# Performance work log

Hardware: AMD Instinct MI355X
Metric: run time of the kernel (lower is better)

The kernel has to match this reference:

```python
import jax, jax.numpy as jnp
import numpy as np
import math

HID = 4096
SLOTS = 8
HEADS = 8
BD = 512  # bottleneck_dim
HD = BD // HEADS  # effective head dim = 64
B, S = 4, 4096


def setup_inputs() -> dict:
    key = jax.random.key(0)
    ks = jax.random.split(key, 8)
    std = 1.0 / math.sqrt(HID)
    return {
        "hidden_states": jax.random.normal(ks[0], (B, S, HID), dtype=jnp.float32),
        "attention_mask": jax.random.randint(ks[1], (B, S), 0, 2, dtype=jnp.int32),
        "memory_slots": jax.random.normal(ks[2], (SLOTS, HID), dtype=jnp.float32) * std,
        # torch nn.Linear weights are [out_features, in_features]
        "Wq": jax.random.normal(ks[3], (BD, HID), dtype=jnp.float32) * std,
        "Wk": jax.random.normal(ks[4], (BD, HID), dtype=jnp.float32) * std,
        "Wv": jax.random.normal(ks[5], (BD, HID), dtype=jnp.float32) * std,
        "Wo": jax.random.normal(ks[6], (HID, BD), dtype=jnp.float32) * (1.0 / math.sqrt(BD)),
    }


def reference(hidden_states, attention_mask, memory_slots, Wq, Wk, Wv, Wo):
    # Q from learnable slots (same for every batch element): [slots, BD]
    Q = memory_slots @ Wq.T
    Q = Q.reshape(SLOTS, HEADS, HD)                      # n h d
    # K/V from sequence: [b, s, BD] -> [b, s, h, d]
    K = jnp.einsum('bsi,oi->bso', hidden_states, Wk).reshape(B, S, HEADS, HD)
    V = jnp.einsum('bsi,oi->bso', hidden_states, Wv).reshape(B, S, HEADS, HD)
    # scores: [b, h, n, s]
    scores = jnp.einsum('nhd,bshd->bhns', Q, K) / jnp.sqrt(jnp.array(HD, scores_dtype := jnp.float32))
    mask = attention_mask[:, None, None, :]              # [b,1,1,s]
    scores = jnp.where(mask == 0, jnp.finfo(scores.dtype).min, scores)
    attn = jax.nn.softmax(scores, axis=-1)
    # output: [b, n, h, d] -> [b, n, BD]
    out = jnp.einsum('bhns,bshd->bnhd', attn, V).reshape(B, SLOTS, BD)
    # o_proj back to hidden_size
    return jnp.einsum('bnd,od->bno', out, Wo)            # [b, slots, HID]
```

## Files before the change

### kernel.cpp

```cpp
#include <hip/hip_runtime.h>
#include <math.h>

#define HID   4096
#define SLOTS 8
#define HEADS 8
#define BD    512
#define HD    64
#define BB    4
#define SS    4096
#define R64   64
#define LSTR  72

typedef __attribute__((ext_vector_type(8))) short bf16x8;
typedef __attribute__((ext_vector_type(4))) float f32x4;

__device__ __forceinline__ unsigned short f2bf(float x) {
  unsigned int u = __builtin_bit_cast(unsigned int, x);
  return (unsigned short)((u + 0x7fffu + ((u >> 16) & 1u)) >> 16);
}

__global__ void q_kernel(const float* __restrict__ ms, const float* __restrict__ Wq,
                         float* __restrict__ Q) {
  int w = (blockIdx.x * blockDim.x + threadIdx.x) >> 6;
  int lane = threadIdx.x & 63;
  if (w >= SLOTS * BD) return;
  int n = w >> 9, o = w & (BD - 1);
  const float* a = ms + n * HID;
  const float* b = Wq + (size_t)o * HID;
  float acc = 0.f;
  for (int i = lane; i < HID; i += 64) acc = fmaf(a[i], b[i], acc);
  #pragma unroll
  for (int off = 32; off; off >>= 1) acc += __shfl_down(acc, off, 64);
  if (lane == 0) Q[w] = acc;
}

__global__ void qw_kernel(const float* __restrict__ Q, const float* __restrict__ Wk,
                          unsigned short* __restrict__ QW) {
  int idx = blockIdx.x * blockDim.x + threadIdx.x;
  int r = idx >> 12, i = idx & (HID - 1);
  int h = r >> 3, n = r & 7;
  const float* q  = Q + n * BD + h * HD;
  const float* wk = Wk + (size_t)(h * HD) * HID + i;
  float acc = 0.f;
  #pragma unroll 8
  for (int d = 0; d < HD; ++d) acc = fmaf(q[d], wk[(size_t)d * HID], acc);
  QW[idx] = f2bf(acc * 0.125f);
}

__global__ __launch_bounds__(256) void scores_mfma(const float* __restrict__ hs,
                                                   const unsigned short* __restrict__ QW,
                                                   float* __restrict__ sp) {
  __shared__ unsigned short As[64 * LSTR];
  __shared__ unsigned short Bs[64 * LSTR];
  const int stile = blockIdx.x, b = blockIdx.y;
  const int tid = threadIdx.x;
  const int wv = tid >> 6, lane = tid & 63;
  const int quad = lane >> 4, l16 = lane & 15;
  const int srow = tid >> 2, kc = (tid & 3) << 4;
  const float* hsp = hs + ((size_t)(b * SS + stile * 64 + srow)) * HID + kc;
  const unsigned short* qwp = QW + (size_t)srow * HID + kc;

  f32x4 acc[4] = {};
  float4 fa0 = *(const float4*)(hsp + 0);
  float4 fa1 = *(const float4*)(hsp + 4);
  float4 fa2 = *(const float4*)(hsp + 8);
  float4 fa3 = *(const float4*)(hsp + 12);
  uint4 qb0 = *(const uint4*)(qwp);
  uint4 qb1 = *(const uint4*)(qwp + 8);

  for (int c = 0; c < 64; ++c) {
    __syncthreads();
    union { unsigned short us[16]; uint4 q[2]; } u;
    float f[16] = {fa0.x, fa0.y, fa0.z, fa0.w, fa1.x, fa1.y, fa1.z, fa1.w,
                   fa2.x, fa2.y, fa2.z, fa2.w, fa3.x, fa3.y, fa3.z, fa3.w};
    #pragma unroll
    for (int j = 0; j < 16; ++j) u.us[j] = f2bf(f[j]);
    *(uint4*)&As[srow * LSTR + kc]     = u.q[0];
    *(uint4*)&As[srow * LSTR + kc + 8] = u.q[1];
    *(uint4*)&Bs[srow * LSTR + kc]     = qb0;
    *(uint4*)&Bs[srow * LSTR + kc + 8] = qb1;
    __syncthreads();
    if (c < 63) {
      const float* p = hsp + (size_t)(c + 1) * 64;
      fa0 = *(const float4*)(p + 0);
      fa1 = *(const float4*)(p + 4);
      fa2 = *(const float4*)(p + 8);
      fa3 = *(const float4*)(p + 12);
      const unsigned short* q = qwp + (size_t)(c + 1) * 64;
      qb0 = *(const uint4*)(q);
      qb1 = *(const uint4*)(q + 8);
    }
    #pragma unroll
    for (int ks = 0; ks < 2; ++ks) {
      bf16x8 bfrag = *(const bf16x8*)&Bs[(wv * 16 + l16) * LSTR + ks * 32 + quad * 8];
      #pragma unroll
      for (int mt = 0; mt < 4; ++mt) {
        bf16x8 afrag = *(const bf16x8*)&As[(mt * 16 + l16) * LSTR + ks * 32 + quad * 8];
        acc[mt] = __builtin_amdgcn_mfma_f32_16x16x32_bf16(afrag, bfrag, acc[mt], 0, 0, 0);
      }
    }
  }
  const int r = wv * 16 + l16;
  #pragma unroll
  for (int mt = 0; mt < 4; ++mt) {
    int s = stile * 64 + mt * 16 + quad * 4;
    float4 v = make_float4(acc[mt][0], acc[mt][1], acc[mt][2], acc[mt][3]);
    *(float4*)(sp + ((size_t)(b * R64 + r)) * SS + s) = v;
  }
}

__global__ __launch_bounds__(256) void softmax_kernel(const float* __restrict__ sp,
                                                      const int* __restrict__ mask,
                                                      unsigned short* __restrict__ attn) {
  int br = blockIdx.x;
  int b = br >> 6;
  int tid = threadIdx.x;
  const float* row = sp + (size_t)br * SS;
  const int* mrow = mask + b * SS;
  float vals[16];
  float mx = -INFINITY;
  #pragma unroll
  for (int j = 0; j < 16; ++j) {
    int s = tid + j * 256;
    float v = row[s];
    if (mrow[s] == 0) v = -INFINITY;
    vals[j] = v;
    mx = fmaxf(mx, v);
  }
  __shared__ float redm[4], reds[4];
  #pragma unroll
  for (int off = 32; off; off >>= 1) mx = fmaxf(mx, __shfl_down(mx, off, 64));
  if ((tid & 63) == 0) redm[tid >> 6] = mx;
  __syncthreads();
  mx = fmaxf(fmaxf(redm[0], redm[1]), fmaxf(redm[2], redm[3]));
  float sum = 0.f;
  #pragma unroll
  for (int j = 0; j < 16; ++j) { vals[j] = expf(vals[j] - mx); sum += vals[j]; }
  #pragma unroll
  for (int off = 32; off; off >>= 1) sum += __shfl_down(sum, off, 64);
  if ((tid & 63) == 0) reds[tid >> 6] = sum;
  __syncthreads();
  sum = reds[0] + reds[1] + reds[2] + reds[3];
  float inv = 1.f / sum;
  #pragma unroll
  for (int j = 0; j < 16; ++j)
    attn[(size_t)br * SS + tid + j * 256] = f2bf(vals[j] * inv);
}

__global__ __launch_bounds__(256) void ctx_mfma(const unsigned short* __restrict__ attn,
                                                const float* __restrict__ hs,
                                                float* __restrict__ ctx) {
  __shared__ unsigned short As[64 * LSTR];
  __shared__ unsigned short Bs[64 * LSTR];
  const int itile = blockIdx.x, b = blockIdx.y;
  const int tid = threadIdx.x;
  const int wv = tid >> 6, lane = tid & 63;
  const int quad = lane >> 4, l16 = lane & 15;
  const int arow = tid >> 2, asc = (tid & 3) << 4;
  const unsigned short* ap = attn + ((size_t)(b * R64 + arow)) * SS + asc;
  const int p = tid & 31, g = tid >> 5;
  const float* bp0 = hs + ((size_t)(b * SS + 2 * p)) * HID + itile * 64 + g * 8;
  const float* bp1 = bp0 + HID;

  f32x4 acc[4] = {};
  uint4 aa0 = *(const uint4*)(ap);
  uint4 aa1 = *(const uint4*)(ap + 8);
  float4 hb00 = *(const float4*)(bp0);
  float4 hb01 = *(const float4*)(bp0 + 4);
  float4 hb10 = *(const float4*)(bp1);
  float4 hb11 = *(const float4*)(bp1 + 4);

  for (int c = 0; c < 64; ++c) {
    __syncthreads();
    *(uint4*)&As[arow * LSTR + asc]     = aa0;
    *(uint4*)&As[arow * LSTR + asc + 8] = aa1;
    {
      float lo[8] = {hb00.x, hb00.y, hb00.z, hb00.w, hb01.x, hb01.y, hb01.z, hb01.w};
      float hi[8] = {hb10.x, hb10.y, hb10.z, hb10.w, hb11.x, hb11.y, hb11.z, hb11.w};
      #pragma unroll
      for (int j = 0; j < 8; ++j) {
        unsigned int v = (unsigned int)f2bf(lo[j]) | ((unsigned int)f2bf(hi[j]) << 16);
        ((unsigned int*)Bs)[(g * 8 + j) * (LSTR / 2) + p] = v;
      }
    }
    __syncthreads();
    if (c < 63) {
      const unsigned short* an = ap + (size_t)(c + 1) * 64;
      aa0 = *(const uint4*)(an);
      aa1 = *(const uint4*)(an + 8);
      const float* bn0 = bp0 + (size_t)(c + 1) * 64 * HID;
      const float* bn1 = bn0 + HID;
      hb00 = *(const float4*)(bn0);
      hb01 = *(const float4*)(bn0 + 4);
      hb10 = *(const float4*)(bn1);
      hb11 = *(const float4*)(bn1 + 4);
    }
    #pragma unroll
    for (int ks = 0; ks < 2; ++ks) {
      bf16x8 bfrag = *(const bf16x8*)&Bs[(wv * 16 + l16) * LSTR + ks * 32 + quad * 8];
      #pragma unroll
      for (int mt = 0; mt < 4; ++mt) {
        bf16x8 afrag = *(const bf16x8*)&As[(mt * 16 + l16) * LSTR + ks * 32 + quad * 8];
        acc[mt] = __builtin_amdgcn_mfma_f32_16x16x32_bf16(afrag, bfrag, acc[mt], 0, 0, 0);
      }
    }
  }
  const int i = itile * 64 + wv * 16 + l16;
  #pragma unroll
  for (int mt = 0; mt < 4; ++mt) {
    int r0 = mt * 16 + quad * 4;
    #pragma unroll
    for (int j = 0; j < 4; ++j)
      ctx[((size_t)(b * R64 + r0 + j)) * HID + i] = acc[mt][j];
  }
}

__global__ void out_kernel(const float* __restrict__ ctx, const float* __restrict__ Wv,
                           float* __restrict__ out) {
  int w = (blockIdx.x * blockDim.x + threadIdx.x) >> 6;
  int lane = threadIdx.x & 63;
  if (w >= BB * SLOTS * BD) return;
  int b = w >> 12, n = (w >> 9) & 7, hd = w & 511, h = hd >> 6;
  const float* c  = ctx + ((size_t)b * R64 + h * 8 + n) * HID;
  const float* wv = Wv + (size_t)hd * HID;
  float acc = 0.f;
  for (int i = lane; i < HID; i += 64) acc = fmaf(c[i], wv[i], acc);
  #pragma unroll
  for (int off = 32; off; off >>= 1) acc += __shfl_down(acc, off, 64);
  if (lane == 0) out[w] = acc;
}

__global__ void final_kernel(const float* __restrict__ out, const float* __restrict__ Wo,
                             float* __restrict__ y) {
  int w = (blockIdx.x * blockDim.x + threadIdx.x) >> 6;
  int lane = threadIdx.x & 63;
  if (w >= BB * SLOTS * HID) return;
  int bn = w >> 12, o = w & 4095;
  const float* orow = out + bn * BD;
  const float* wo = Wo + (size_t)o * BD;
  float acc = 0.f;
  #pragma unroll
  for (int d = lane; d < BD; d += 64) acc = fmaf(orow[d], wo[d], acc);
  #pragma unroll
  for (int off = 32; off; off >>= 1) acc += __shfl_down(acc, off, 64);
  if (lane == 0) y[w] = acc;
}

extern "C" void kernel_launch(void* const* d_in, const int* in_sizes, int n_in,
                              void* d_out, int out_size, void* d_ws, size_t ws_size,
                              hipStream_t stream) {
  const float* hs   = (const float*)d_in[0];
  const int*   mask = (const int*)d_in[1];
  const float* ms   = (const float*)d_in[2];
  const float* Wq   = (const float*)d_in[3];
  const float* Wk   = (const float*)d_in[4];
  const float* Wv   = (const float*)d_in[5];
  const float* Wo   = (const float*)d_in[6];

  char* ws = (char*)d_ws;
  float*          Q    = (float*)ws;                    ws += 4096 * 4;
  unsigned short* QW   = (unsigned short*)ws;           ws += R64 * HID * 2;
  float*          sp   = (float*)ws;                    ws += (size_t)BB * R64 * SS * 4;
  unsigned short* attn = (unsigned short*)ws;           ws += (size_t)BB * R64 * SS * 2;
  float*          ctx  = (float*)ws;                    ws += (size_t)BB * R64 * HID * 4;
  float*          out  = (float*)ws;

  q_kernel<<<dim3((SLOTS * BD * 64) / 256), 256, 0, stream>>>(ms, Wq, Q);
  qw_kernel<<<dim3((R64 * HID) / 256), 256, 0, stream>>>(Q, Wk, QW);
  scores_mfma<<<dim3(64, 4), 256, 0, stream>>>(hs, QW, sp);
  softmax_kernel<<<dim3(BB * R64), 256, 0, stream>>>(sp, mask, attn);
  ctx_mfma<<<dim3(64, 4), 256, 0, stream>>>(attn, hs, ctx);
  out_kernel<<<dim3(4096), 256, 0, stream>>>(ctx, Wv, out);
  final_kernel<<<dim3(32768), 256, 0, stream>>>(out, Wo, (float*)d_out);
}
```

Measured before the change: 580.9 us.

## Split-K the scores and context GEMMs and reuse weights in projection kernels

Splits the reduction dimension of both MFMA GEMMs into four chunks via a z grid dimension, growing each grid from 256 to 1024 blocks so more of the GPU's CUs are busy. Partial scores are summed inside the softmax, and partial contexts are summed in a new reduction kernel. The out and final projection kernels are restructured so each weight row is loaded once and reused across 8 slots and 32 rows, instead of being reloaded per output. The cost is extra workspace and the memory traffic for the partial buffers, plus one more kernel launch.

```diff
diff --git a/kernel.cpp b/kernel.cpp
--- a/kernel.cpp
+++ b/kernel.cpp
@@ -10,6 +10,8 @@
 #define SS    4096
 #define R64   64
 #define LSTR  72
+#define KC    1024
+#define NKZ   4
 
 typedef __attribute__((ext_vector_type(8))) short bf16x8;
 typedef __attribute__((ext_vector_type(4))) float f32x4;
@@ -52,13 +54,13 @@
                                                    float* __restrict__ sp) {
   __shared__ unsigned short As[64 * LSTR];
   __shared__ unsigned short Bs[64 * LSTR];
-  const int stile = blockIdx.x, b = blockIdx.y;
+  const int stile = blockIdx.x, b = blockIdx.y, kz = blockIdx.z;
   const int tid = threadIdx.x;
   const int wv = tid >> 6, lane = tid & 63;
   const int quad = lane >> 4, l16 = lane & 15;
   const int srow = tid >> 2, kc = (tid & 3) << 4;
-  const float* hsp = hs + ((size_t)(b * SS + stile * 64 + srow)) * HID + kc;
-  const unsigned short* qwp = QW + (size_t)srow * HID + kc;
+  const float* hsp = hs + ((size_t)(b * SS + stile * 64 + srow)) * HID + kz * KC + kc;
+  const unsigned short* qwp = QW + (size_t)srow * HID + kz * KC + kc;
 
   f32x4 acc[4] = {};
   float4 fa0 = *(const float4*)(hsp + 0);
@@ -68,7 +70,7 @@
   uint4 qb0 = *(const uint4*)(qwp);
   uint4 qb1 = *(const uint4*)(qwp + 8);
 
-  for (int c = 0; c < 64; ++c) {
+  for (int c = 0; c < 16; ++c) {
     __syncthreads();
     union { unsigned short us[16]; uint4 q[2]; } u;
     float f[16] = {fa0.x, fa0.y, fa0.z, fa0.w, fa1.x, fa1.y, fa1.z, fa1.w,
@@ -80,7 +82,7 @@
     *(uint4*)&Bs[srow * LSTR + kc]     = qb0;
     *(uint4*)&Bs[srow * LSTR + kc + 8] = qb1;
     __syncthreads();
-    if (c < 63) {
+    if (c < 15) {
       const float* p = hsp + (size_t)(c + 1) * 64;
       fa0 = *(const float4*)(p + 0);
       fa1 = *(const float4*)(p + 4);
@@ -105,7 +107,7 @@
   for (int mt = 0; mt < 4; ++mt) {
     int s = stile * 64 + mt * 16 + quad * 4;
     float4 v = make_float4(acc[mt][0], acc[mt][1], acc[mt][2], acc[mt][3]);
-    *(float4*)(sp + ((size_t)(b * R64 + r)) * SS + s) = v;
+    *(float4*)(sp + ((size_t)((kz * BB + b) * R64 + r)) * SS + s) = v;
   }
 }
 
@@ -115,14 +117,17 @@
   int br = blockIdx.x;
   int b = br >> 6;
   int tid = threadIdx.x;
-  const float* row = sp + (size_t)br * SS;
+  const float* p0 = sp + ((size_t)(0 * BB * R64) + br) * SS;
+  const float* p1 = sp + ((size_t)(1 * BB * R64) + br) * SS;
+  const float* p2 = sp + ((size_t)(2 * BB * R64) + br) * SS;
+  const float* p3 = sp + ((size_t)(3 * BB * R64) + br) * SS;
   const int* mrow = mask + b * SS;
   float vals[16];
   float mx = -INFINITY;
   #pragma unroll
   for (int j = 0; j < 16; ++j) {
     int s = tid + j * 256;
-    float v = row[s];
+    float v = p0[s] + p1[s] + p2[s] + p3[s];
     if (mrow[s] == 0) v = -INFINITY;
     vals[j] = v;
     mx = fmaxf(mx, v);
@@ -149,17 +154,17 @@
 
 __global__ __launch_bounds__(256) void ctx_mfma(const unsigned short* __restrict__ attn,
                                                 const float* __restrict__ hs,
-                                                float* __restrict__ ctx) {
+                                                float* __restrict__ ctxp) {
   __shared__ unsigned short As[64 * LSTR];
   __shared__ unsigned short Bs[64 * LSTR];
-  const int itile = blockIdx.x, b = blockIdx.y;
+  const int itile = blockIdx.x, b = blockIdx.y, kz = blockIdx.z;
   const int tid = threadIdx.x;
   const int wv = tid >> 6, lane = tid & 63;
   const int quad = lane >> 4, l16 = lane & 15;
   const int arow = tid >> 2, asc = (tid & 3) << 4;
-  const unsigned short* ap = attn + ((size_t)(b * R64 + arow)) * SS + asc;
+  const unsigned short* ap = attn + ((size_t)(b * R64 + arow)) * SS + kz * KC + asc;
   const int p = tid & 31, g = tid >> 5;
-  const float* bp0 = hs + ((size_t)(b * SS + 2 * p)) * HID + itile * 64 + g * 8;
+  const float* bp0 = hs + ((size_t)(b * SS + kz * KC + 2 * p)) * HID + itile * 64 + g * 8;
   const float* bp1 = bp0 + HID;
 
   f32x4 acc[4] = {};
@@ -170,7 +175,7 @@
   float4 hb10 = *(const float4*)(bp1);
   float4 hb11 = *(const float4*)(bp1 + 4);
 
-  for (int c = 0; c < 64; ++c) {
+  for (int c = 0; c < 16; ++c) {
     __syncthreads();
     *(uint4*)&As[arow * LSTR + asc]     = aa0;
     *(uint4*)&As[arow * LSTR + asc + 8] = aa1;
@@ -184,7 +189,7 @@
       }
     }
     __syncthreads();
-    if (c < 63) {
+    if (c < 15) {
       const unsigned short* an = ap + (size_t)(c + 1) * 64;
       aa0 = *(const uint4*)(an);
       aa1 = *(const uint4*)(an + 8);
@@ -211,39 +216,65 @@
     int r0 = mt * 16 + quad * 4;
     #pragma unroll
     for (int j = 0; j < 4; ++j)
-      ctx[((size_t)(b * R64 + r0 + j)) * HID + i] = acc[mt][j];
-  }
+      ctxp[((size_t)((kz * BB + b) * R64 + r0 + j)) * HID + i] = acc[mt][j];
+  }
+}
+
+__global__ void ctxsum_kernel(const float* __restrict__ ctxp, float* __restrict__ ctxs) {
+  int idx = blockIdx.x * blockDim.x + threadIdx.x;
+  const size_t n4 = (size_t)BB * R64 * HID / 4;
+  if ((size_t)idx >= n4) return;
+  const float4* a = (const float4*)ctxp;
+  float4 v0 = a[idx];
+  float4 v1 = a[idx + n4];
+  float4 v2 = a[idx + 2 * n4];
+  float4 v3 = a[idx + 3 * n4];
+  float4 r = make_float4(v0.x + v1.x + v2.x + v3.x, v0.y + v1.y + v2.y + v3.y,
+                         v0.z + v1.z + v2.z + v3.z, v0.w + v1.w + v2.w + v3.w);
+  ((float4*)ctxs)[idx] = r;
 }
 
 __global__ void out_kernel(const float* __restrict__ ctx, const float* __restrict__ Wv,
                            float* __restrict__ out) {
   int w = (blockIdx.x * blockDim.x + threadIdx.x) >> 6;
   int lane = threadIdx.x & 63;
-  if (w >= BB * SLOTS * BD) return;
-  int b = w >> 12, n = (w >> 9) & 7, hd = w & 511, h = hd >> 6;
-  const float* c  = ctx + ((size_t)b * R64 + h * 8 + n) * HID;
-  const float* wv = Wv + (size_t)hd * HID;
-  float acc = 0.f;
-  for (int i = lane; i < HID; i += 64) acc = fmaf(c[i], wv[i], acc);
-  #pragma unroll
-  for (int off = 32; off; off >>= 1) acc += __shfl_down(acc, off, 64);
-  if (lane == 0) out[w] = acc;
+  if (w >= BB * BD) return;
+  int b = w >> 9, hd = w & 511, h = hd >> 6;
+  const float* wvp = Wv + (size_t)hd * HID;
+  const float* cb  = ctx + ((size_t)b * R64 + h * 8) * HID;
+  float acc[8] = {};
+  for (int i = lane; i < HID; i += 64) {
+    float wv = wvp[i];
+    #pragma unroll
+    for (int n = 0; n < 8; ++n) acc[n] = fmaf(cb[(size_t)n * HID + i], wv, acc[n]);
+  }
+  #pragma unroll
+  for (int n = 0; n < 8; ++n) {
+    float a = acc[n];
+    #pragma unroll
+    for (int off = 32; off; off >>= 1) a += __shfl_down(a, off, 64);
+    if (lane == 0) out[((size_t)(b * SLOTS + n)) * BD + hd] = a;
+  }
 }
 
 __global__ void final_kernel(const float* __restrict__ out, const float* __restrict__ Wo,
                              float* __restrict__ y) {
   int w = (blockIdx.x * blockDim.x + threadIdx.x) >> 6;
   int lane = threadIdx.x & 63;
-  if (w >= BB * SLOTS * HID) return;
-  int bn = w >> 12, o = w & 4095;
-  const float* orow = out + bn * BD;
-  const float* wo = Wo + (size_t)o * BD;
-  float acc = 0.f;
-  #pragma unroll
-  for (int d = lane; d < BD; d += 64) acc = fmaf(orow[d], wo[d], acc);
-  #pragma unroll
-  for (int off = 32; off; off >>= 1) acc += __shfl_down(acc, off, 64);
-  if (lane == 0) y[w] = acc;
+  if (w >= HID) return;
+  const float* wo = Wo + (size_t)w * BD;
+  float wreg[8];
+  #pragma unroll
+  for (int j = 0; j < 8; ++j) wreg[j] = wo[lane + j * 64];
+  for (int bn = 0; bn < BB * SLOTS; ++bn) {
+    const float* orow = out + bn * BD;
+    float acc = 0.f;
+    #pragma unroll
+    for (int j = 0; j < 8; ++j) acc = fmaf(orow[lane + j * 64], wreg[j], acc);
+    #pragma unroll
+    for (int off = 32; off; off >>= 1) acc += __shfl_down(acc, off, 64);
+    if (lane == 0) y[(size_t)bn * HID + w] = acc;
+  }
 }
 
 extern "C" void kernel_launch(void* const* d_in, const int* in_sizes, int n_in,
@@ -258,18 +289,20 @@
   const float* Wo   = (const float*)d_in[6];
 
   char* ws = (char*)d_ws;
-  float*          Q    = (float*)ws;                    ws += 4096 * 4;
-  unsigned short* QW   = (unsigned short*)ws;           ws += R64 * HID * 2;
-  float*          sp   = (float*)ws;                    ws += (size_t)BB * R64 * SS * 4;
-  unsigned short* attn = (unsigned short*)ws;           ws += (size_t)BB * R64 * SS * 2;
-  float*          ctx  = (float*)ws;                    ws += (size_t)BB * R64 * HID * 4;
+  float*          Q    = (float*)ws;          ws += 4096 * 4;
+  unsigned short* QW   = (unsigned short*)ws; ws += R64 * HID * 2;
+  float*          sp   = (float*)ws;          ws += (size_t)NKZ * BB * R64 * SS * 4;
+  unsigned short* attn = (unsigned short*)ws; ws += (size_t)BB * R64 * SS * 2;
+  float*          ctxp = (float*)ws;          ws += (size_t)NKZ * BB * R64 * HID * 4;
+  float*          ctxs = (float*)ws;          ws += (size_t)BB * R64 * HID * 4;
   float*          out  = (float*)ws;
 
   q_kernel<<<dim3((SLOTS * BD * 64) / 256), 256, 0, stream>>>(ms, Wq, Q);
   qw_kernel<<<dim3((R64 * HID) / 256), 256, 0, stream>>>(Q, Wk, QW);
-  scores_mfma<<<dim3(64, 4), 256, 0, stream>>>(hs, QW, sp);
+  scores_mfma<<<dim3(64, 4, 4), 256, 0, stream>>>(hs, QW, sp);
   softmax_kernel<<<dim3(BB * R64), 256, 0, stream>>>(sp, mask, attn);
-  ctx_mfma<<<dim3(64, 4), 256, 0, stream>>>(attn, hs, ctx);
-  out_kernel<<<dim3(4096), 256, 0, stream>>>(ctx, Wv, out);
-  final_kernel<<<dim3(32768), 256, 0, stream>>>(out, Wo, (float*)d_out);
-}
+  ctx_mfma<<<dim3(64, 4, 4), 256, 0, stream>>>(attn, hs, ctxp);
+  ctxsum_kernel<<<dim3((BB * R64 * HID / 4) / 256), 256, 0, stream>>>(ctxp, ctxs);
+  out_kernel<<<dim3((BB * BD * 64) / 256), 256, 0, stream>>>(ctxs, Wv, out);
+  final_kernel<<<dim3((HID * 64) / 256), 256, 0, stream>>>(out, Wo, (float*)d_out);
+}
```

After: 566.1 us. 2.6% less time.
